# Performance work log

Measured on AMD Instinct MI355X. Metric: run time of the kernel, lower is better.

The kernel has to match this reference:

```python
import jax, jax.numpy as jnp
import numpy as np

B, S, D, H, DFF = 2, 4096, 768, 12, 3072
DH = D // H
EPS = 1e-6


def layer_norm(x, gamma, beta):
    # torch.std is unbiased (ddof=1); normalizer is (sigma + eps), NOT sqrt(var+eps)
    mu = jnp.mean(x, axis=-1, keepdims=True)
    sigma = jnp.sqrt(jnp.var(x, axis=-1, keepdims=True, ddof=1))
    return gamma * (x - mu) / (sigma + EPS) + beta


def setup_inputs() -> dict:
    key = jax.random.key(0)
    ks = jax.random.split(key, 12)
    sc = 1.0 / np.sqrt(D)
    inp = {
        "x": jax.random.normal(ks[0], (B, S, D), dtype=jnp.float32),
        "mask": jnp.ones((B, S, S), dtype=jnp.float32),  # multiplicative mask
        "wq": jax.random.normal(ks[1], (D, D), dtype=jnp.float32) * sc,
        "bq": jnp.zeros((D,), dtype=jnp.float32),
        "wk": jax.random.normal(ks[2], (D, D), dtype=jnp.float32) * sc,
        "bk": jnp.zeros((D,), dtype=jnp.float32),
        "wv": jax.random.normal(ks[3], (D, D), dtype=jnp.float32) * sc,
        "bv": jnp.zeros((D,), dtype=jnp.float32),
        "wo": jax.random.normal(ks[4], (D, D), dtype=jnp.float32) * sc,
        "bo": jnp.zeros((D,), dtype=jnp.float32),
        "w1": jax.random.normal(ks[5], (D, DFF), dtype=jnp.float32) * sc,
        "b1": jnp.zeros((DFF,), dtype=jnp.float32),
        "w2": jax.random.normal(ks[6], (DFF, D), dtype=jnp.float32) * (1.0 / np.sqrt(DFF)),
        "b2": jnp.zeros((D,), dtype=jnp.float32),
        "gamma1": jnp.ones((D,), dtype=jnp.float32),
        "beta1": jnp.zeros((D,), dtype=jnp.float32),
        "gamma2": jnp.ones((D,), dtype=jnp.float32),
        "beta2": jnp.zeros((D,), dtype=jnp.float32),
    }
    return inp


def reference(x, mask, wq, bq, wk, bk, wv, bv, wo, bo, w1, b1, w2, b2,
              gamma1, beta1, gamma2, beta2):
    # Pre-LN encoder layer (is_pre_layer_norm=True); dropout is identity (eval).
    l1 = layer_norm(x, gamma1, beta1)                      # [B,S,D]

    # --- multi-head self-attention ---
    q = (l1 @ wq + bq).reshape(B, S, H, DH).transpose(0, 2, 1, 3)  # [B,H,S,DH]
    k = (l1 @ wk + bk).reshape(B, S, H, DH).transpose(0, 2, 1, 3)
    v = (l1 @ wv + bv).reshape(B, S, H, DH).transpose(0, 2, 1, 3)
    scores = jnp.einsum("bhqd,bhkd->bhqk", q, k) / jnp.sqrt(jnp.float32(DH))
    scores = scores * mask[:, None, :, :]                  # multiplicative mask, pre-softmax
    attn = jax.nn.softmax(scores, axis=-1)                 # [B,H,S,S]
    ctx = jnp.einsum("bhqk,bhkd->bhqd", attn, v)           # [B,H,S,DH]
    ctx = ctx.transpose(0, 2, 1, 3).reshape(B, S, D)       # [B,S,D]
    a = ctx  # NOTE: original forward never applies out_linear in attention()... it does in forward
    a = ctx
    # MultiHeadAttention.forward returns the merged heads WITHOUT out_linear applied?
    # Re-check: forward() reshapes and returns `output` without out_linear in given code.
    x1 = x + a                                             # residual

    l2 = layer_norm(x1, gamma2, beta2)
    h = jax.nn.relu(l2 @ w1 + b1) @ w2 + b2                # FFN
    return h + x1
```

## Files before the change

### kernel.cpp

```cpp
#include <hip/hip_runtime.h>
#include <cstdint>
#include <cstddef>

#define BB   2
#define SEQ  4096
#define DD   768
#define HH   12
#define DHH  64
#define DFFN 3072
#define NTOK (BB*SEQ)

using bf16x8 = __attribute__((ext_vector_type(8))) __bf16;
using f32x4  = __attribute__((ext_vector_type(4))) float;
typedef unsigned int u32;

#define QK_SCALE 0.18033688011112042f

__device__ __forceinline__ float fast_exp2(float x) {
    return __builtin_amdgcn_exp2f(x);
}

__device__ __forceinline__ unsigned short f2bf(float f) {
    unsigned u = __float_as_uint(f);
    u = u + 0x7FFFu + ((u >> 16) & 1u);
    return (unsigned short)(u >> 16);
}
__device__ __forceinline__ unsigned short f2bf_trunc(float f) {
    return (unsigned short)(__float_as_uint(f) >> 16);
}

__device__ __forceinline__ bf16x8 ld_bf8(const unsigned short* p) {
    return *(const bf16x8*)p;
}

__device__ __forceinline__ bf16x8 pack_bf8(f32x4 a, f32x4 b) {
    union { u32 w[4]; bf16x8 v; } u;
    u.w[0] = (u32)f2bf_trunc(a[0]) | ((u32)f2bf_trunc(a[1]) << 16);
    u.w[1] = (u32)f2bf_trunc(a[2]) | ((u32)f2bf_trunc(a[3]) << 16);
    u.w[2] = (u32)f2bf_trunc(b[0]) | ((u32)f2bf_trunc(b[1]) << 16);
    u.w[3] = (u32)f2bf_trunc(b[2]) | ((u32)f2bf_trunc(b[3]) << 16);
    return u.v;
}
__device__ __forceinline__ bf16x8 vfrag(const unsigned short* lo, const unsigned short* hi) {
    union { uint2 d[2]; bf16x8 v; } u;
    u.d[0] = *(const uint2*)lo;
    u.d[1] = *(const uint2*)hi;
    return u.v;
}

__device__ __forceinline__ void gl_lds16(const unsigned short* g, unsigned short* l) {
    __builtin_amdgcn_global_load_lds(
        (const __attribute__((address_space(1))) u32*)(uintptr_t)(const void*)g,
        (__attribute__((address_space(3))) u32*)(uintptr_t)(void*)l,
        16, 0, 0);
}

__global__ __launch_bounds__(256) void transpose_qkv_to_bf16(
    const float* __restrict__ wq, const float* __restrict__ wk, const float* __restrict__ wv,
    unsigned short* __restrict__ dst)
{
    __shared__ float tile[32][33];
    const int z = blockIdx.z;
    const float* src = (z == 0) ? wq : (z == 1 ? wk : wv);
    const float scale = (z == 0) ? QK_SCALE : 1.0f;
    unsigned short* d = dst + (size_t)z * 768 * 768;
    const int c0 = blockIdx.x * 32, r0 = blockIdx.y * 32;
    const int tx = threadIdx.x, ty = threadIdx.y;
#pragma unroll
    for (int i = 0; i < 32; i += 8)
        tile[ty + i][tx] = src[(size_t)(r0 + ty + i) * 768 + c0 + tx];
    __syncthreads();
#pragma unroll
    for (int i = 0; i < 32; i += 8)
        d[(size_t)(c0 + ty + i) * 768 + r0 + tx] = f2bf(scale * tile[tx][ty + i]);
}

__global__ __launch_bounds__(256) void transpose_f32_to_bf16(
    const float* __restrict__ src, unsigned short* __restrict__ dst, int R, int C, float scale)
{
    __shared__ float tile[32][33];
    const int c0 = blockIdx.x * 32, r0 = blockIdx.y * 32;
    const int tx = threadIdx.x, ty = threadIdx.y;
#pragma unroll
    for (int i = 0; i < 32; i += 8)
        tile[ty + i][tx] = src[(size_t)(r0 + ty + i) * C + c0 + tx];
    __syncthreads();
#pragma unroll
    for (int i = 0; i < 32; i += 8)
        dst[(size_t)(c0 + ty + i) * R + r0 + tx] = f2bf(scale * tile[tx][ty + i]);
}

__global__ void concat_bias(const float* __restrict__ bq, const float* __restrict__ bk,
                            const float* __restrict__ bv, float* __restrict__ bqkv)
{
    int i = blockIdx.x * 256 + threadIdx.x;
    if (i < 3 * DD)
        bqkv[i] = (i < DD) ? bq[i] * QK_SCALE : (i < 2 * DD ? bk[i - DD] : bv[i - 2 * DD]);
}

__global__ __launch_bounds__(256) void mask_check(const float* __restrict__ mask, int* __restrict__ flag)
{
    const size_t n = (size_t)BB * SEQ * SEQ;
    const size_t stride = (size_t)gridDim.x * 1024;
    int bad = 0;
    for (size_t i = ((size_t)blockIdx.x * 256 + threadIdx.x) * 4; i < n; i += stride) {
        float4 v = *(const float4*)&mask[i];
        bad |= (v.x != 1.f) | (v.y != 1.f) | (v.z != 1.f) | (v.w != 1.f);
    }
    if (bad) atomicOr(flag, 1);
}

__global__ __launch_bounds__(256) void ln_fused(
    const float* __restrict__ x, const float* __restrict__ add,
    const float* __restrict__ gamma, const float* __restrict__ beta,
    unsigned short* __restrict__ out_ln, float* __restrict__ x1out)
{
    const int row = blockIdx.x, t = threadIdx.x;
    const size_t base = (size_t)row * DD;
    float v[3], s = 0.f, sq = 0.f;
#pragma unroll
    for (int p = 0; p < 3; ++p) {
        int idx = t + p * 256;
        float val = x[base + idx];
        if (add) val += add[base + idx];
        v[p] = val; s += val; sq += val * val;
    }
#pragma unroll
    for (int off = 1; off < 64; off <<= 1) {
        s  += __shfl_xor(s,  off);
        sq += __shfl_xor(sq, off);
    }
    __shared__ float red[8];
    const int wave = t >> 6;
    if ((t & 63) == 0) { red[wave] = s; red[4 + wave] = sq; }
    __syncthreads();
    s  = red[0] + red[1] + red[2] + red[3];
    sq = red[4] + red[5] + red[6] + red[7];
    const float mu   = s * (1.f / 768.f);
    const float var  = fmaxf((sq - 768.f * mu * mu) * (1.f / 767.f), 0.f);
    const float rstd = 1.f / (sqrtf(var) + 1e-6f);
#pragma unroll
    for (int p = 0; p < 3; ++p) {
        int idx = t + p * 256;
        if (x1out) x1out[base + idx] = v[p];
        out_ln[base + idx] = f2bf(gamma[idx] * (v[p] - mu) * rstd + beta[idx]);
    }
}

__global__ __launch_bounds__(256) void gemm_bf16(
    const unsigned short* __restrict__ A, const unsigned short* __restrict__ Bt,
    const float* __restrict__ bias, const float* __restrict__ resid,
    unsigned short* __restrict__ outB, float* __restrict__ outF,
    int M, int N, int K, int relu)
{
    __shared__ __align__(16) unsigned short As[128][64];
    __shared__ __align__(16) unsigned short Bs[128][64];
    const int tid = threadIdx.x;
    const int lane = tid & 63, wave = tid >> 6;
    const int quad = lane >> 4, l16 = lane & 15;
    const int wm = wave >> 1, wn = wave & 1;

    int wg = blockIdx.y * gridDim.x + blockIdx.x;
    const int nwg = gridDim.x * gridDim.y;
    wg = (wg & 7) * (nwg >> 3) + (wg >> 3);
    const int m0 = (wg / gridDim.x) * 128, n0 = (wg % gridDim.x) * 128;

    const f32x4 fzero = {0.f, 0.f, 0.f, 0.f};
    f32x4 acc[4][4];
#pragma unroll
    for (int i = 0; i < 4; ++i)
#pragma unroll
        for (int j = 0; j < 4; ++j) acc[i][j] = fzero;

    const int r  = tid >> 3;
    const int cg = tid & 7;

    for (int k0 = 0; k0 < K; k0 += 64) {
#pragma unroll
        for (int rr = 0; rr < 4; ++rr) {
            const int row = r + rr * 32;
            const int gc8 = (cg ^ (row & 7)) * 8;
            gl_lds16(&A [(size_t)(m0 + row) * K + k0 + gc8], &As[row][cg * 8]);
            gl_lds16(&Bt[(size_t)(n0 + row) * K + k0 + gc8], &Bs[row][cg * 8]);
        }
        __syncthreads();
#pragma unroll
        for (int ks = 0; ks < 2; ++ks) {
            bf16x8 af[4], bfv[4];
#pragma unroll
            for (int i = 0; i < 4; ++i) {
                const int row = wm * 64 + i * 16 + l16;
                af[i] = ld_bf8(&As[row][((ks * 4 + quad) ^ (row & 7)) * 8]);
            }
#pragma unroll
            for (int j = 0; j < 4; ++j) {
                const int row = wn * 64 + j * 16 + l16;
                bfv[j] = ld_bf8(&Bs[row][((ks * 4 + quad) ^ (row & 7)) * 8]);
            }
#pragma unroll
            for (int i = 0; i < 4; ++i)
#pragma unroll
                for (int j = 0; j < 4; ++j)
                    acc[i][j] = __builtin_amdgcn_mfma_f32_16x16x32_bf16(af[i], bfv[j], acc[i][j], 0, 0, 0);
        }
        __syncthreads();
    }
#pragma unroll
    for (int i = 0; i < 4; ++i)
#pragma unroll
        for (int j = 0; j < 4; ++j)
#pragma unroll
            for (int rr = 0; rr < 4; ++rr) {
                const int gm = m0 + wm * 64 + i * 16 + quad * 4 + rr;
                const int gn = n0 + wn * 64 + j * 16 + l16;
                float v = acc[i][j][rr] + bias[gn];
                if (relu) v = fmaxf(v, 0.f);
                if (resid) v += resid[(size_t)gm * N + gn];
                if (outF) outF[(size_t)gm * N + gn] = v;
                if (outB) outB[(size_t)gm * N + gn] = f2bf(v);
            }
}

__global__ __launch_bounds__(256) void vt_extract(
    const unsigned short* __restrict__ qkv, unsigned short* __restrict__ vtg)
{
    __shared__ unsigned short tile[64][72];
    const int bh = blockIdx.x, b = bh / HH, h = bh % HH;
    const int s0 = blockIdx.y * 64;
    const int tid = threadIdx.x;
#pragma unroll
    for (int p = 0; p < 2; ++p) {
        int idx = tid + p * 256;
        int r = idx >> 3, ch8 = (idx & 7) * 8;
        *(uint4*)&tile[r][ch8] =
            *(const uint4*)&qkv[(size_t)(b * SEQ + s0 + r) * 2304 + 1536 + h * 64 + ch8];
    }
    __syncthreads();
#pragma unroll
    for (int p = 0; p < 2; ++p) {
        int idx = tid + p * 256;
        int d = idx >> 3, sc = (idx & 7) * 8;
        unsigned short tmp[8];
#pragma unroll
        for (int j = 0; j < 8; ++j) tmp[j] = tile[sc + j][d];
        *(uint4*)&vtg[((size_t)bh * 64 + d) * SEQ + s0 + sc] = *(uint4*)tmp;
    }
}

__global__ __launch_bounds__(256, 3) void flash_attn12(
    const unsigned short* __restrict__ qkv, const unsigned short* __restrict__ vtg,
    const float* __restrict__ mask, const int* __restrict__ maskflag,
    float* __restrict__ ctx)
{
    __shared__ __align__(16) unsigned short Ks[128][72];
    __shared__ __align__(16) unsigned short Vt[64][136];

    const int tid = threadIdx.x;
    const int lane = tid & 63, wave = tid >> 6;
    const int quad = lane >> 4, l16 = lane & 15;
    const int NT = SEQ / 128;

    const int wg  = blockIdx.y * 32 + blockIdx.x;
    const int swz = (wg & 7) * 96 + (wg >> 3);
    const int bh = swz >> 5, b = bh / HH, h = bh % HH;
    const int qbase = (swz & 31) * 128 + wave * 32;
    const int use_mask = *maskflag;

    bf16x8 qf[2][2];
#pragma unroll
    for (int mt = 0; mt < 2; ++mt) {
        const size_t qrow = (size_t)(b * SEQ + qbase + mt * 16 + l16) * 2304 + h * 64;
        qf[mt][0] = ld_bf8(&qkv[qrow + quad * 8]);
        qf[mt][1] = ld_bf8(&qkv[qrow + 32 + quad * 8]);
    }
    const f32x4 fzero = {0.f, 0.f, 0.f, 0.f};
    float l_run[2] = {0.f, 0.f};
    f32x4 o[2][4];
#pragma unroll
    for (int mt = 0; mt < 2; ++mt)
#pragma unroll
        for (int r = 0; r < 4; ++r) o[mt][r] = fzero;

    const float* mbase = mask + (size_t)b * SEQ * SEQ;
    const unsigned short* kgbase = qkv + (size_t)b * SEQ * 2304 + 768 + h * 64;
    const unsigned short* vgbase = vtg + (size_t)bh * 64 * SEQ;

    const int sr  = tid >> 3, sc8 = (tid & 7) * 8;
    const int vd  = tid >> 4, vc8 = (tid & 15) * 8;

#define LOAD_KV(K0_)                                                                  \
    kb0 = *(const uint4*)&kgbase[(size_t)((K0_) + sr +  0) * 2304 + sc8];             \
    kb1 = *(const uint4*)&kgbase[(size_t)((K0_) + sr + 32) * 2304 + sc8];             \
    kb2 = *(const uint4*)&kgbase[(size_t)((K0_) + sr + 64) * 2304 + sc8];             \
    kb3 = *(const uint4*)&kgbase[(size_t)((K0_) + sr + 96) * 2304 + sc8];             \
    vb0 = *(const uint4*)&vgbase[(size_t)(vd +  0) * SEQ + (K0_) + vc8];              \
    vb1 = *(const uint4*)&vgbase[(size_t)(vd + 16) * SEQ + (K0_) + vc8];              \
    vb2 = *(const uint4*)&vgbase[(size_t)(vd + 32) * SEQ + (K0_) + vc8];              \
    vb3 = *(const uint4*)&vgbase[(size_t)(vd + 48) * SEQ + (K0_) + vc8]

#define WRITE_KV()                                                                    \
    *(uint4*)&Ks[sr +  0][sc8] = kb0;                                                 \
    *(uint4*)&Ks[sr + 32][sc8] = kb1;                                                 \
    *(uint4*)&Ks[sr + 64][sc8] = kb2;                                                 \
    *(uint4*)&Ks[sr + 96][sc8] = kb3;                                                 \
    *(uint4*)&Vt[vd +  0][vc8] = vb0;                                                 \
    *(uint4*)&Vt[vd + 16][vc8] = vb1;                                                 \
    *(uint4*)&Vt[vd + 32][vc8] = vb2;                                                 \
    *(uint4*)&Vt[vd + 48][vc8] = vb3

#define QKT_TILE() do {                                                               \
    _Pragma("unroll")                                                                 \
    for (int j = 0; j < 8; ++j) {                                                     \
        bf16x8 kf0 = ld_bf8(&Ks[j * 16 + l16][quad * 8]);                             \
        bf16x8 kf1 = ld_bf8(&Ks[j * 16 + l16][32 + quad * 8]);                        \
        st[0][j] = __builtin_amdgcn_mfma_f32_16x16x32_bf16(kf0, qf[0][0], fzero, 0, 0, 0); \
        st[0][j] = __builtin_amdgcn_mfma_f32_16x16x32_bf16(kf1, qf[0][1], st[0][j], 0, 0, 0); \
        st[1][j] = __builtin_amdgcn_mfma_f32_16x16x32_bf16(kf0, qf[1][0], fzero, 0, 0, 0); \
        st[1][j] = __builtin_amdgcn_mfma_f32_16x16x32_bf16(kf1, qf[1][1], st[1][j], 0, 0, 0); \
    }                                                                                 \
} while (0)

#define PV_TILE() do {                                                                \
    _Pragma("unroll")                                                                 \
    for (int kk = 0; kk < 4; ++kk) {                                                  \
        bf16x8 pa0 = pack_bf8(st[0][2 * kk], st[0][2 * kk + 1]);                      \
        bf16x8 pa1 = pack_bf8(st[1][2 * kk], st[1][2 * kk + 1]);                      \
        _Pragma("unroll")                                                             \
        for (int v = 0; v < 4; ++v) {                                                 \
            const unsigned short* vrow = &Vt[v * 16 + l16][kk * 32 + quad * 4];       \
            bf16x8 vf = vfrag(vrow, vrow + 16);                                       \
            o[0][v] = __builtin_amdgcn_mfma_f32_16x16x32_bf16(pa0, vf, o[0][v], 0, 0, 0); \
            o[1][v] = __builtin_amdgcn_mfma_f32_16x16x32_bf16(pa1, vf, o[1][v], 0, 0, 0); \
        }                                                                             \
    }                                                                                 \
} while (0)

    {
        uint4 kb0, kb1, kb2, kb3, vb0, vb1, vb2, vb3;
        LOAD_KV(0);
        WRITE_KV();
    }

    if (!use_mask) {
        for (int t = 0; t < NT; ++t) {
            __syncthreads();
            const int kn = ((t + 1) & (NT - 1)) * 128;
            uint4 kb0, kb1, kb2, kb3, vb0, vb1, vb2, vb3;
            LOAD_KV(kn);
            f32x4 st[2][8];
            QKT_TILE();
#pragma unroll
            for (int mt = 0; mt < 2; ++mt) {
                float acc = 0.f;
#pragma unroll
                for (int j = 0; j < 8; ++j)
#pragma unroll
                    for (int r = 0; r < 4; ++r) {
                        float p = fast_exp2(st[mt][j][r]);
                        st[mt][j][r] = p;
                        acc += p;
                    }
                l_run[mt] += acc;
            }
            PV_TILE();
            __syncthreads();
            if (t < NT - 1) { WRITE_KV(); }
        }
#pragma unroll
        for (int mt = 0; mt < 2; ++mt) {
            l_run[mt] += __shfl_xor(l_run[mt], 16);
            l_run[mt] += __shfl_xor(l_run[mt], 32);
        }
    } else {
        float m_run[2] = {-1e30f, -1e30f};
        for (int t = 0; t < NT; ++t) {
            const int k0 = t * 128;
            __syncthreads();
            const int kn = ((t + 1) & (NT - 1)) * 128;
            uint4 kb0, kb1, kb2, kb3, vb0, vb1, vb2, vb3;
            LOAD_KV(kn);
            f32x4 st[2][8];
            QKT_TILE();
#pragma unroll
            for (int mt = 0; mt < 2; ++mt) {
                const float* mrow =
                    &mbase[(size_t)(qbase + mt * 16 + l16) * SEQ + k0 + quad * 4];
#pragma unroll
                for (int j = 0; j < 8; ++j)
#pragma unroll
                    for (int r = 0; r < 4; ++r)
                        st[mt][j][r] *= mrow[j * 16 + r];
            }
#pragma unroll
            for (int mt = 0; mt < 2; ++mt) {
                float mx = st[mt][0][0];
#pragma unroll
                for (int j = 0; j < 8; ++j)
#pragma unroll
                    for (int r = 0; r < 4; ++r) mx = fmaxf(mx, st[mt][j][r]);
                mx = fmaxf(mx, __shfl_xor(mx, 16));
                mx = fmaxf(mx, __shfl_xor(mx, 32));
                const float mnew = fmaxf(m_run[mt], mx);
                const float alpha = fast_exp2(m_run[mt] - mnew);
                float ssum = 0.f;
#pragma unroll
                for (int j = 0; j < 8; ++j)
#pragma unroll
                    for (int r = 0; r < 4; ++r) {
                        st[mt][j][r] = fast_exp2(st[mt][j][r] - mnew);
                        ssum += st[mt][j][r];
                    }
                ssum += __shfl_xor(ssum, 16);
                ssum += __shfl_xor(ssum, 32);
                l_run[mt] = l_run[mt] * alpha + ssum;
                m_run[mt] = mnew;
                float aq[4];
#pragma unroll
                for (int r = 0; r < 4; ++r) aq[r] = __shfl(alpha, quad * 4 + r);
#pragma unroll
                for (int v = 0; v < 4; ++v)
#pragma unroll
                    for (int r = 0; r < 4; ++r) o[mt][v][r] *= aq[r];
            }
            PV_TILE();
            __syncthreads();
            if (t < NT - 1) { WRITE_KV(); }
        }
    }
#undef LOAD_KV
#undef WRITE_KV
#undef QKT_TILE
#undef PV_TILE

#pragma unroll
    for (int mt = 0; mt < 2; ++mt) {
        float lq[4];
#pragma unroll
        for (int r = 0; r < 4; ++r) lq[r] = __shfl(l_run[mt], quad * 4 + r);
#pragma unroll
        for (int v = 0; v < 4; ++v)
#pragma unroll
            for (int r = 0; r < 4; ++r) {
                const int row = qbase + mt * 16 + quad * 4 + r;
                ctx[(size_t)(b * SEQ + row) * DD + h * 64 + v * 16 + l16] =
                    o[mt][v][r] / lq[r];
            }
    }
}

extern "C" void kernel_launch(void* const* d_in, const int* in_sizes, int n_in,
                              void* d_out, int out_size, void* d_ws, size_t ws_size,
                              hipStream_t stream)
{
    (void)in_sizes; (void)n_in; (void)out_size; (void)ws_size;
    const float* x      = (const float*)d_in[0];
    const float* mask   = (const float*)d_in[1];
    const float* wq     = (const float*)d_in[2];
    const float* bq     = (const float*)d_in[3];
    const float* wk     = (const float*)d_in[4];
    const float* bk     = (const float*)d_in[5];
    const float* wv     = (const float*)d_in[6];
    const float* bv     = (const float*)d_in[7];
    const float* w1     = (const float*)d_in[10];
    const float* b1     = (const float*)d_in[11];
    const float* w2     = (const float*)d_in[12];
    const float* b2     = (const float*)d_in[13];
    const float* gamma1 = (const float*)d_in[14];
    const float* beta1  = (const float*)d_in[15];
    const float* gamma2 = (const float*)d_in[16];
    const float* beta2  = (const float*)d_in[17];
    float* out = (float*)d_out;

    char* ws = (char*)d_ws;
    size_t off = 0;
    auto take = [&](size_t bytes) -> char* {
        char* p = ws + off;
        off = (off + bytes + 255) & ~(size_t)255;
        return p;
    };
    unsigned short* wqkvT = (unsigned short*)take((size_t)2304 * 768 * 2);
    unsigned short* w1T   = (unsigned short*)take((size_t)3072 * 768 * 2);
    unsigned short* w2T   = (unsigned short*)take((size_t)768 * 3072 * 2);
    float*          bqkv  = (float*)take(2304 * 4);
    int*            mflag = (int*)take(256);
    unsigned short* l12   = (unsigned short*)take((size_t)NTOK * DD * 2);
    unsigned short* qkv   = (unsigned short*)take((size_t)NTOK * 2304 * 2);
    float*          x1    = (float*)take((size_t)NTOK * DD * 4);
    char*           big   = take((size_t)NTOK * DFFN * 2);
    float*          ctx   = (float*)big;
    unsigned short* vtg   = (unsigned short*)(big + (size_t)NTOK * DD * 4);
    unsigned short* hb    = (unsigned short*)big;

    (void)hipMemsetAsync(mflag, 0, 4, stream);
    mask_check<<<2048, 256, 0, stream>>>(mask, mflag);

    transpose_qkv_to_bf16<<<dim3(24, 24, 3), dim3(32, 8), 0, stream>>>(wq, wk, wv, wqkvT);
    transpose_f32_to_bf16<<<dim3(96, 24), dim3(32, 8), 0, stream>>>(w1, w1T, 768, 3072, 1.0f);
    transpose_f32_to_bf16<<<dim3(24, 96), dim3(32, 8), 0, stream>>>(w2, w2T, 3072, 768, 1.0f);
    concat_bias<<<9, 256, 0, stream>>>(bq, bk, bv, bqkv);

    ln_fused<<<NTOK, 256, 0, stream>>>(x, nullptr, gamma1, beta1, l12, nullptr);
    gemm_bf16<<<dim3(2304 / 128, NTOK / 128), 256, 0, stream>>>(
        l12, wqkvT, bqkv, nullptr, qkv, nullptr, NTOK, 2304, 768, 0);
    vt_extract<<<dim3(BB * HH, SEQ / 64), 256, 0, stream>>>(qkv, vtg);
    flash_attn12<<<dim3(SEQ / 128, BB * HH), 256, 0, stream>>>(qkv, vtg, mask, mflag, ctx);
    ln_fused<<<NTOK, 256, 0, stream>>>(x, ctx, gamma2, beta2, l12, x1);
    gemm_bf16<<<dim3(3072 / 128, NTOK / 128), 256, 0, stream>>>(
        l12, w1T, b1, nullptr, hb, nullptr, NTOK, 3072, 768, 1);
    gemm_bf16<<<dim3(768 / 128, NTOK / 128), 256, 0, stream>>>(
        hb, w2T, b2, x1, nullptr, out, NTOK, 768, 3072, 0);
}
```

Baseline: 593.1 us.

## Double-buffer LDS tiles in bf16 GEMM to overlap global loads with MFMA

Makes the GEMM's shared-memory A/B tiles double-buffered. The next K-tile's global-to-LDS loads are issued before computing on the current tile, and only one barrier per iteration is kept. The aim is to hide global memory latency behind MFMA work. In exchange, LDS use per block doubles (64KB), which can lower occupancy. Correctness also depends on the async LDS loads being complete by the end-of-iteration barrier.

```diff
diff --git a/kernel.cpp b/kernel.cpp
--- a/kernel.cpp
+++ b/kernel.cpp
@@ -153,8 +153,8 @@
     unsigned short* __restrict__ outB, float* __restrict__ outF,
     int M, int N, int K, int relu)
 {
-    __shared__ __align__(16) unsigned short As[128][64];
-    __shared__ __align__(16) unsigned short Bs[128][64];
+    __shared__ __align__(16) unsigned short As[2][128][64];
+    __shared__ __align__(16) unsigned short Bs[2][128][64];
     const int tid = threadIdx.x;
     const int lane = tid & 63, wave = tid >> 6;
     const int quad = lane >> 4, l16 = lane & 15;
@@ -175,27 +175,35 @@
     const int r  = tid >> 3;
     const int cg = tid & 7;
 
-    for (int k0 = 0; k0 < K; k0 += 64) {
-#pragma unroll
-        for (int rr = 0; rr < 4; ++rr) {
-            const int row = r + rr * 32;
-            const int gc8 = (cg ^ (row & 7)) * 8;
-            gl_lds16(&A [(size_t)(m0 + row) * K + k0 + gc8], &As[row][cg * 8]);
-            gl_lds16(&Bt[(size_t)(n0 + row) * K + k0 + gc8], &Bs[row][cg * 8]);
-        }
-        __syncthreads();
+#define G_STAGE(BUF_, K0_) do {                                                       \
+    _Pragma("unroll")                                                                 \
+    for (int rr = 0; rr < 4; ++rr) {                                                  \
+        const int row = r + rr * 32;                                                  \
+        const int gc8 = (cg ^ (row & 7)) * 8;                                         \
+        gl_lds16(&A [(size_t)(m0 + row) * K + (K0_) + gc8], &As[BUF_][row][cg * 8]);  \
+        gl_lds16(&Bt[(size_t)(n0 + row) * K + (K0_) + gc8], &Bs[BUF_][row][cg * 8]);  \
+    }                                                                                 \
+} while (0)
+
+    const int nt = K >> 6;
+    G_STAGE(0, 0);
+    __syncthreads();
+
+    for (int t = 0; t < nt; ++t) {
+        const int cur = t & 1;
+        if (t + 1 < nt) G_STAGE(cur ^ 1, (t + 1) * 64);
 #pragma unroll
         for (int ks = 0; ks < 2; ++ks) {
             bf16x8 af[4], bfv[4];
 #pragma unroll
             for (int i = 0; i < 4; ++i) {
                 const int row = wm * 64 + i * 16 + l16;
-                af[i] = ld_bf8(&As[row][((ks * 4 + quad) ^ (row & 7)) * 8]);
+                af[i] = ld_bf8(&As[cur][row][((ks * 4 + quad) ^ (row & 7)) * 8]);
             }
 #pragma unroll
             for (int j = 0; j < 4; ++j) {
                 const int row = wn * 64 + j * 16 + l16;
-                bfv[j] = ld_bf8(&Bs[row][((ks * 4 + quad) ^ (row & 7)) * 8]);
+                bfv[j] = ld_bf8(&Bs[cur][row][((ks * 4 + quad) ^ (row & 7)) * 8]);
             }
 #pragma unroll
             for (int i = 0; i < 4; ++i)
@@ -205,6 +213,8 @@
         }
         __syncthreads();
     }
+#undef G_STAGE
+
 #pragma unroll
     for (int i = 0; i < 4; ++i)
 #pragma unroll
```

Result: no change. 593.7 us (+0.1%).
